# Kernel tuning notes

Hardware: AMD Instinct MI355X
Metric: run time of the kernel (lower is better)

## Reference

```python
import jax, jax.numpy as jnp
import numpy as np

BATCH, HID, STEPS = 64, 2048, 30

def setup_inputs() -> dict:
    key = jax.random.key(0)
    ks = jax.random.split(key, 7)
    s = 1.0 / np.sqrt(HID)  # pytorch LSTM/Linear init scale
    return {
        "monthly_token": jax.random.normal(ks[0], (BATCH, HID), jnp.float32),
        "steps": STEPS,
        "W_ih": jax.random.uniform(ks[1], (4 * HID, HID), jnp.float32, -s, s),
        "W_hh": jax.random.uniform(ks[2], (4 * HID, HID), jnp.float32, -s, s),
        "b_ih": jax.random.uniform(ks[3], (4 * HID,), jnp.float32, -s, s),
        "b_hh": jax.random.uniform(ks[4], (4 * HID,), jnp.float32, -s, s),
        "W_out": jax.random.uniform(ks[5], (1, HID), jnp.float32, -s, s),
        "b_out": jax.random.uniform(ks[6], (1,), jnp.float32, -s, s),
    }

def reference(monthly_token, steps, W_ih, W_hh, b_ih, b_hh, W_out, b_out):
    H = monthly_token.shape[1]
    h0 = monthly_token                      # (B, H) initial hidden
    c0 = jnp.zeros_like(h0)
    x0 = jnp.zeros_like(h0)                 # first lstm input is zeros

    def step(carry, _):
        h, c, x = carry
        # PyTorch gate order: input, forget, cell(g), output
        gates = x @ W_ih.T + b_ih + h @ W_hh.T + b_hh   # (B, 4H)
        i, f, g, o = jnp.split(gates, 4, axis=-1)
        i = jax.nn.sigmoid(i)
        f = jax.nn.sigmoid(f)
        g = jnp.tanh(g)
        o = jax.nn.sigmoid(o)
        c_new = f * c + i * g
        h_new = o * jnp.tanh(c_new)
        y = h_new @ W_out.T + b_out          # (B, 1) daily value
        # feedback: next input is the lstm output (= h_new for 1-layer LSTM)
        return (h_new, c_new, h_new), y[:, 0]

    _, ys = jax.lax.scan(step, (h0, c0, x0), xs=None, length=steps)
    return ys.T                               # (B, steps)
```

## Files before the change

### kernel.cpp

```cpp
#include <hip/hip_runtime.h>
#include <cmath>


#define HID   2048
#define BATCH 64
#define G4    8192
#define NCU   256
#define HGRP  (HID * BATCH / 8)
#define NFLAGS 512

typedef __attribute__((ext_vector_type(8))) _Float16 half8;
typedef __attribute__((ext_vector_type(4))) float f32x4;

#define LDS_BYTES 155648

__global__ void k_init(const float* __restrict__ token, const float* __restrict__ bih,
                       const float* __restrict__ bhh, half8* __restrict__ h0p,
                       float* __restrict__ bsum, unsigned* __restrict__ flags) {
    int g = blockIdx.x * 256 + threadIdx.x;
    int l = g & 63, nt = (g >> 6) & 3, kt = g >> 8;
    int n = nt * 16 + (l & 15);
    int k0 = kt * 32 + (l >> 4) * 8;
    const float4* ps = (const float4*)(token + (size_t)n * HID + k0);
    float4 a = ps[0], b = ps[1];
    half8 v;
    v[0]=(_Float16)a.x; v[1]=(_Float16)a.y; v[2]=(_Float16)a.z; v[3]=(_Float16)a.w;
    v[4]=(_Float16)b.x; v[5]=(_Float16)b.y; v[6]=(_Float16)b.z; v[7]=(_Float16)b.w;
    h0p[g] = v;
    if (g < G4) bsum[g] = bih[g] + bhh[g];
    if (g < NFLAGS) flags[g] = 0u;
}

__global__ __launch_bounds__(512, 2)
void k_lstm(const float* __restrict__ wih, const float* __restrict__ whh,
            const float* __restrict__ bsum, const float* __restrict__ wout,
            _Float16* __restrict__ hbuf,
            float* __restrict__ ypart,
            unsigned* __restrict__ flags, int steps) {
    extern __shared__ char smem[];
    half8* Wlds = (half8*)smem;
    f32x4* red4 = (f32x4*)(smem + 131072);

    const int tid  = threadIdx.x;
    const int blk  = blockIdx.x;
    const int lane = tid & 63;
    const int w    = tid >> 6;
    const int half = w & 1;
    const int ks   = w >> 1;
    const int q    = lane >> 4;
    const int col  = lane & 15;

    for (int idx = tid; idx < 2 * 64 * 64; idx += 512) {
        int l = idx & 63, kt = (idx >> 6) & 63, m2 = idx >> 12;
        int m = l & 15;
        int gate = m2 * 2 + (m >> 3);
        int row  = gate * HID + blk * 8 + (m & 7);
        int colw = kt * 32 + (l >> 4) * 8;
        const float4* p = (const float4*)(whh + (size_t)row * HID + colw);
        float4 a = p[0], b = p[1];
        half8 v;
        v[0]=(_Float16)a.x; v[1]=(_Float16)a.y; v[2]=(_Float16)a.z; v[3]=(_Float16)a.w;
        v[4]=(_Float16)b.x; v[5]=(_Float16)b.y; v[6]=(_Float16)b.z; v[7]=(_Float16)b.w;
        Wlds[idx] = v;
    }

    float biasA[4] = {0,0,0,0}, biasB[4] = {0,0,0,0}, wj4[4] = {0,0,0,0};
    float c4[4] = {0.0f, 0.0f, 0.0f, 0.0f};
    if (w < 2) {
        #pragma unroll
        for (int r = 0; r < 4; ++r) {
            int rA = 4 * q + r;
            int rB = 16 + 4 * q + r;
            biasA[r] = bsum[(rA >> 3) * HID + blk * 8 + (rA & 7)];
            biasB[r] = bsum[(rB >> 3) * HID + blk * 8 + (rB & 7)];
            wj4[r]   = wout[blk * 8 + (q & 1) * 4 + r];
        }
    }
    __syncthreads();

    for (int t = 0; t < steps; ++t) {
        if (t) {
            while (__hip_atomic_load(&flags[half * NCU + ks * 64 + lane],
                                     __ATOMIC_RELAXED, __HIP_MEMORY_SCOPE_AGENT)
                   < (unsigned)t)
                __builtin_amdgcn_s_sleep(1);
            asm volatile("" ::: "memory");
        }
        const half8* hp = (const half8*)(hbuf + (size_t)t * HID * BATCH);
        f32x4 a00 = {0,0,0,0}, a01 = {0,0,0,0}, a10 = {0,0,0,0}, a11 = {0,0,0,0};
        const int ktb = ks * 16;
        #pragma unroll
        for (int kk = 0; kk < 16; ++kk) {
            int kt = ktb + kk;
            half8 av0 = Wlds[(kt) * 64 + lane];
            half8 av1 = Wlds[(64 + kt) * 64 + lane];
            half8 b0  = hp[(kt * 4 + half * 2 + 0) * 64 + lane];
            half8 b1  = hp[(kt * 4 + half * 2 + 1) * 64 + lane];
            a00 = __builtin_amdgcn_mfma_f32_16x16x32_f16(av0, b0, a00, 0, 0, 0);
            a01 = __builtin_amdgcn_mfma_f32_16x16x32_f16(av0, b1, a01, 0, 0, 0);
            a10 = __builtin_amdgcn_mfma_f32_16x16x32_f16(av1, b0, a10, 0, 0, 0);
            a11 = __builtin_amdgcn_mfma_f32_16x16x32_f16(av1, b1, a11, 0, 0, 0);
        }
        if (ks == 1 || ks == 3) {
            int srow = (ks == 3 ? 2 : 0) + half;
            red4[(srow * 4 + 0) * 64 + lane] = a00;
            red4[(srow * 4 + 1) * 64 + lane] = a01;
            red4[(srow * 4 + 2) * 64 + lane] = a10;
            red4[(srow * 4 + 3) * 64 + lane] = a11;
        }
        __syncthreads();
        if (ks == 0) {
            int srow = half;
            a00 += red4[(srow * 4 + 0) * 64 + lane];
            a01 += red4[(srow * 4 + 1) * 64 + lane];
            a10 += red4[(srow * 4 + 2) * 64 + lane];
            a11 += red4[(srow * 4 + 3) * 64 + lane];
        } else if (ks == 2) {
            int srow = 2 + half;
            a00 += red4[(srow * 4 + 0) * 64 + lane];
            a01 += red4[(srow * 4 + 1) * 64 + lane];
            a10 += red4[(srow * 4 + 2) * 64 + lane];
            a11 += red4[(srow * 4 + 3) * 64 + lane];
            int sdst = 4 + half;
            red4[(sdst * 4 + 0) * 64 + lane] = a00;
            red4[(sdst * 4 + 1) * 64 + lane] = a01;
            red4[(sdst * 4 + 2) * 64 + lane] = a10;
            red4[(sdst * 4 + 3) * 64 + lane] = a11;
        }
        __syncthreads();
        if (w < 2) {
            int srow = 4 + half;
            a00 += red4[(srow * 4 + 0) * 64 + lane];
            a01 += red4[(srow * 4 + 1) * 64 + lane];
            a10 += red4[(srow * 4 + 2) * 64 + lane];
            a11 += red4[(srow * 4 + 3) * 64 + lane];
            #pragma unroll
            for (int r = 0; r < 4; ++r) {
                a00[r] += biasA[r]; a01[r] += biasA[r];
                a10[r] += biasB[r]; a11[r] += biasB[r];
            }
            float x00[4], x01[4], x10[4], x11[4];
            #pragma unroll
            for (int r = 0; r < 4; ++r) {
                x00[r] = __shfl_xor(a00[r], 32);
                x01[r] = __shfl_xor(a01[r], 32);
                x10[r] = __shfl_xor(a10[r], 32);
                x11[r] = __shfl_xor(a11[r], 32);
            }
            const bool lo = (lane < 32);
            float hv[4];
            #pragma unroll
            for (int r = 0; r < 4; ++r) {
                float gi = lo ? a00[r] : x01[r];
                float gf = lo ? x00[r] : a01[r];
                float gg = lo ? a10[r] : x11[r];
                float go = lo ? x10[r] : a11[r];
                float iv = 1.0f / (1.0f + __expf(-gi));
                float fv = 1.0f / (1.0f + __expf(-gf));
                float eg = __expf(2.0f * gg);
                float gv = 1.0f - 2.0f / (eg + 1.0f);
                float ov = 1.0f / (1.0f + __expf(-go));
                c4[r] = fv * c4[r] + iv * gv;
                float ec = __expf(2.0f * c4[r]);
                float th = 1.0f - 2.0f / (ec + 1.0f);
                hv[r] = ov * th;
            }
            if (t < steps - 1) {
                union { unsigned short us[4]; unsigned long long ull; } pk;
                #pragma unroll
                for (int r = 0; r < 4; ++r) {
                    _Float16 hf = (_Float16)hv[r];
                    pk.us[r] = *(unsigned short*)&hf;
                }
                const int nt = half * 2 + (q >> 1);
                const size_t g = (size_t)((blk >> 2) * 4 + nt) * 64
                               + (blk & 3) * 16 + col;
                unsigned long long* dst = (unsigned long long*)
                    (hbuf + (size_t)(t + 1) * HID * BATCH + g * 8) + (q & 1);
                __hip_atomic_store(dst, pk.ull, __ATOMIC_RELAXED,
                                   __HIP_MEMORY_SCOPE_AGENT);
                asm volatile("s_waitcnt vmcnt(0)" ::: "memory");
                if (lane == 0)
                    __hip_atomic_store(&flags[half * NCU + blk], (unsigned)(t + 1),
                                       __ATOMIC_RELAXED, __HIP_MEMORY_SCOPE_AGENT);
            }
            float yp = wj4[0] * hv[0] + wj4[1] * hv[1]
                     + wj4[2] * hv[2] + wj4[3] * hv[3];
            yp += __shfl_xor(yp, 16);
            if ((q & 1) == 0)
                ypart[((size_t)t * NCU + blk) * 64
                      + half * 32 + (q >> 1) * 16 + col] = yp;
        }
        if (t == 0) {
            for (int idx = tid; idx < 2 * 64 * 64; idx += 512) {
                int l = idx & 63, kt = (idx >> 6) & 63, m2 = idx >> 12;
                int m = l & 15;
                int gate = m2 * 2 + (m >> 3);
                int row  = gate * HID + blk * 8 + (m & 7);
                int colw = kt * 32 + (l >> 4) * 8;
                const float4* p = (const float4*)(wih + (size_t)row * HID + colw);
                float4 a = p[0], b = p[1];
                half8 v = Wlds[idx];
                v[0] = (_Float16)((float)v[0] + a.x); v[1] = (_Float16)((float)v[1] + a.y);
                v[2] = (_Float16)((float)v[2] + a.z); v[3] = (_Float16)((float)v[3] + a.w);
                v[4] = (_Float16)((float)v[4] + b.x); v[5] = (_Float16)((float)v[5] + b.y);
                v[6] = (_Float16)((float)v[6] + b.z); v[7] = (_Float16)((float)v[7] + b.w);
                Wlds[idx] = v;
            }
            __syncthreads();
        }
    }
}

__global__ __launch_bounds__(512)
void k_yout(const float* __restrict__ ypart, const float* __restrict__ bout,
            float* __restrict__ out, int steps) {
    __shared__ float red[8][64];
    int t = blockIdx.x;
    int tid = threadIdx.x;
    int b = tid & 63, ch = tid >> 6;
    const float* p = ypart + (size_t)t * NCU * 64 + b;
    float s = 0.0f;
    #pragma unroll 8
    for (int cu = ch * 32; cu < ch * 32 + 32; ++cu) s += p[(size_t)cu * 64];
    red[ch][b] = s;
    __syncthreads();
    if (tid < 64) {
        float r = bout[0];
        #pragma unroll
        for (int u = 0; u < 8; ++u) r += red[u][tid];
        out[(size_t)tid * steps + t] = r;
    }
}

extern "C" void kernel_launch(void* const* d_in, const int* in_sizes, int n_in,
                              void* d_out, int out_size, void* d_ws, size_t ws_size,
                              hipStream_t stream) {
    const float* token = (const float*)d_in[0];
    const float* wih   = (const float*)d_in[2];
    const float* whh   = (const float*)d_in[3];
    const float* bih   = (const float*)d_in[4];
    const float* bhh   = (const float*)d_in[5];
    const float* wout  = (const float*)d_in[6];
    const float* bout  = (const float*)d_in[7];
    float* out = (float*)d_out;
    const int steps = out_size / BATCH;

    char* ws = (char*)d_ws;
    size_t off = 0;
    auto carve = [&](size_t bytes) -> void* {
        void* p = ws + off;
        off = (off + bytes + 255) & ~(size_t)255;
        return p;
    };
    _Float16* hbuf  = (_Float16*)carve((size_t)(steps + 1) * HID * BATCH * 2);
    float*    bsum  = (float*)carve((size_t)G4 * 4);
    float*    ypart = (float*)carve((size_t)steps * NCU * 64 * 4);
    unsigned* flags = (unsigned*)carve(NFLAGS * 4);

    hipFuncSetAttribute(reinterpret_cast<const void*>(&k_lstm),
                        hipFuncAttributeMaxDynamicSharedMemorySize, LDS_BYTES);

    k_init<<<dim3(HGRP / 256), dim3(256), 0, stream>>>(
        token, bih, bhh, (half8*)hbuf, bsum, flags);

    k_lstm<<<dim3(NCU), dim3(512), LDS_BYTES, stream>>>(
        wih, whh, bsum, wout, hbuf, ypart, flags, steps);

    k_yout<<<dim3(steps), dim3(512), 0, stream>>>(ypart, bout, out, steps);
}
```

Baseline: 457.0 us.

## Double workgroup to 1024 threads with gate-interleaved rows and per-wave batch tiles

Raises the persistent LSTM kernel from 8 to 16 waves per block. Each wave now owns one 16-column batch tile, and the W_hh/W_ih rows are re-laid-out in LDS so the four gates of a hidden unit sit in adjacent accumulator rows. This removes the cross-half shuffles in the gate math, lets each wave prefetch all its h fragments before the MFMA loop, and spreads the step's work over more waves to cut per-step latency. In exchange the flag array doubles, more waves poll flags each step, and the h store becomes a shuffle-assembled 32-bit write per lane.

```diff
diff --git a/kernel.cpp b/kernel.cpp
--- a/kernel.cpp
+++ b/kernel.cpp
@@ -7,7 +7,7 @@
 #define G4    8192
 #define NCU   256
 #define HGRP  (HID * BATCH / 8)
-#define NFLAGS 512
+#define NFLAGS 1024
 
 typedef __attribute__((ext_vector_type(8))) _Float16 half8;
 typedef __attribute__((ext_vector_type(4))) float f32x4;
@@ -31,7 +31,7 @@
     if (g < NFLAGS) flags[g] = 0u;
 }
 
-__global__ __launch_bounds__(512, 2)
+__global__ __launch_bounds__(1024, 4)
 void k_lstm(const float* __restrict__ wih, const float* __restrict__ whh,
             const float* __restrict__ bsum, const float* __restrict__ wout,
             _Float16* __restrict__ hbuf,
@@ -45,16 +45,17 @@
     const int blk  = blockIdx.x;
     const int lane = tid & 63;
     const int w    = tid >> 6;
-    const int half = w & 1;
-    const int ks   = w >> 1;
+    const int nt   = w & 3;
+    const int ks   = w >> 2;
     const int q    = lane >> 4;
     const int col  = lane & 15;
 
-    for (int idx = tid; idx < 2 * 64 * 64; idx += 512) {
-        int l = idx & 63, kt = (idx >> 6) & 63, m2 = idx >> 12;
-        int m = l & 15;
-        int gate = m2 * 2 + (m >> 3);
-        int row  = gate * HID + blk * 8 + (m & 7);
+    for (int idx = tid; idx < 2 * 64 * 64; idx += 1024) {
+        int l = idx & 63, kt = (idx >> 6) & 63, mt = idx >> 12;
+        int m16  = l & 15;
+        int gate = m16 & 3;
+        int uloc = (mt ? 4 : 0) + (m16 >> 2);
+        int row  = gate * HID + blk * 8 + uloc;
         int colw = kt * 32 + (l >> 4) * 8;
         const float4* p = (const float4*)(whh + (size_t)row * HID + colw);
         float4 a = p[0], b = p[1];
@@ -64,139 +65,115 @@
         Wlds[idx] = v;
     }
 
-    float biasA[4] = {0,0,0,0}, biasB[4] = {0,0,0,0}, wj4[4] = {0,0,0,0};
-    float c4[4] = {0.0f, 0.0f, 0.0f, 0.0f};
-    if (w < 2) {
+    float bias0[4] = {0,0,0,0}, bias1[4] = {0,0,0,0};
+    float wj0 = 0.0f, wj1 = 0.0f, c20 = 0.0f, c21 = 0.0f;
+    if (ks == 0) {
         #pragma unroll
         for (int r = 0; r < 4; ++r) {
-            int rA = 4 * q + r;
-            int rB = 16 + 4 * q + r;
-            biasA[r] = bsum[(rA >> 3) * HID + blk * 8 + (rA & 7)];
-            biasB[r] = bsum[(rB >> 3) * HID + blk * 8 + (rB & 7)];
-            wj4[r]   = wout[blk * 8 + (q & 1) * 4 + r];
-        }
+            bias0[r] = bsum[r * HID + blk * 8 + q];
+            bias1[r] = bsum[r * HID + blk * 8 + 4 + q];
+        }
+        wj0 = wout[blk * 8 + q];
+        wj1 = wout[blk * 8 + 4 + q];
     }
     __syncthreads();
 
     for (int t = 0; t < steps; ++t) {
         if (t) {
-            while (__hip_atomic_load(&flags[half * NCU + ks * 64 + lane],
+            while (__hip_atomic_load(&flags[nt * NCU + ks * 64 + lane],
                                      __ATOMIC_RELAXED, __HIP_MEMORY_SCOPE_AGENT)
                    < (unsigned)t)
                 __builtin_amdgcn_s_sleep(1);
             asm volatile("" ::: "memory");
         }
         const half8* hp = (const half8*)(hbuf + (size_t)t * HID * BATCH);
-        f32x4 a00 = {0,0,0,0}, a01 = {0,0,0,0}, a10 = {0,0,0,0}, a11 = {0,0,0,0};
         const int ktb = ks * 16;
+        half8 bfr[16];
+        #pragma unroll
+        for (int kk = 0; kk < 16; ++kk)
+            bfr[kk] = hp[((ktb + kk) * 4 + nt) * 64 + lane];
+        __builtin_amdgcn_sched_barrier(0);
+        f32x4 a0 = {0,0,0,0}, a1 = {0,0,0,0};
         #pragma unroll
         for (int kk = 0; kk < 16; ++kk) {
             int kt = ktb + kk;
             half8 av0 = Wlds[(kt) * 64 + lane];
             half8 av1 = Wlds[(64 + kt) * 64 + lane];
-            half8 b0  = hp[(kt * 4 + half * 2 + 0) * 64 + lane];
-            half8 b1  = hp[(kt * 4 + half * 2 + 1) * 64 + lane];
-            a00 = __builtin_amdgcn_mfma_f32_16x16x32_f16(av0, b0, a00, 0, 0, 0);
-            a01 = __builtin_amdgcn_mfma_f32_16x16x32_f16(av0, b1, a01, 0, 0, 0);
-            a10 = __builtin_amdgcn_mfma_f32_16x16x32_f16(av1, b0, a10, 0, 0, 0);
-            a11 = __builtin_amdgcn_mfma_f32_16x16x32_f16(av1, b1, a11, 0, 0, 0);
-        }
-        if (ks == 1 || ks == 3) {
-            int srow = (ks == 3 ? 2 : 0) + half;
-            red4[(srow * 4 + 0) * 64 + lane] = a00;
-            red4[(srow * 4 + 1) * 64 + lane] = a01;
-            red4[(srow * 4 + 2) * 64 + lane] = a10;
-            red4[(srow * 4 + 3) * 64 + lane] = a11;
+            a0 = __builtin_amdgcn_mfma_f32_16x16x32_f16(av0, bfr[kk], a0, 0, 0, 0);
+            a1 = __builtin_amdgcn_mfma_f32_16x16x32_f16(av1, bfr[kk], a1, 0, 0, 0);
+        }
+        if (ks == 1) {
+            red4[(nt * 2 + 0) * 64 + lane] = a0;
+            red4[(nt * 2 + 1) * 64 + lane] = a1;
+        } else if (ks == 3) {
+            red4[(8 + nt * 2 + 0) * 64 + lane] = a0;
+            red4[(8 + nt * 2 + 1) * 64 + lane] = a1;
         }
         __syncthreads();
         if (ks == 0) {
-            int srow = half;
-            a00 += red4[(srow * 4 + 0) * 64 + lane];
-            a01 += red4[(srow * 4 + 1) * 64 + lane];
-            a10 += red4[(srow * 4 + 2) * 64 + lane];
-            a11 += red4[(srow * 4 + 3) * 64 + lane];
+            a0 += red4[(nt * 2 + 0) * 64 + lane];
+            a1 += red4[(nt * 2 + 1) * 64 + lane];
         } else if (ks == 2) {
-            int srow = 2 + half;
-            a00 += red4[(srow * 4 + 0) * 64 + lane];
-            a01 += red4[(srow * 4 + 1) * 64 + lane];
-            a10 += red4[(srow * 4 + 2) * 64 + lane];
-            a11 += red4[(srow * 4 + 3) * 64 + lane];
-            int sdst = 4 + half;
-            red4[(sdst * 4 + 0) * 64 + lane] = a00;
-            red4[(sdst * 4 + 1) * 64 + lane] = a01;
-            red4[(sdst * 4 + 2) * 64 + lane] = a10;
-            red4[(sdst * 4 + 3) * 64 + lane] = a11;
+            a0 += red4[(8 + nt * 2 + 0) * 64 + lane];
+            a1 += red4[(8 + nt * 2 + 1) * 64 + lane];
+            red4[(16 + nt * 2 + 0) * 64 + lane] = a0;
+            red4[(16 + nt * 2 + 1) * 64 + lane] = a1;
         }
         __syncthreads();
-        if (w < 2) {
-            int srow = 4 + half;
-            a00 += red4[(srow * 4 + 0) * 64 + lane];
-            a01 += red4[(srow * 4 + 1) * 64 + lane];
-            a10 += red4[(srow * 4 + 2) * 64 + lane];
-            a11 += red4[(srow * 4 + 3) * 64 + lane];
+        if (ks == 0) {
+            a0 += red4[(16 + nt * 2 + 0) * 64 + lane];
+            a1 += red4[(16 + nt * 2 + 1) * 64 + lane];
             #pragma unroll
-            for (int r = 0; r < 4; ++r) {
-                a00[r] += biasA[r]; a01[r] += biasA[r];
-                a10[r] += biasB[r]; a11[r] += biasB[r];
-            }
-            float x00[4], x01[4], x10[4], x11[4];
-            #pragma unroll
-            for (int r = 0; r < 4; ++r) {
-                x00[r] = __shfl_xor(a00[r], 32);
-                x01[r] = __shfl_xor(a01[r], 32);
-                x10[r] = __shfl_xor(a10[r], 32);
-                x11[r] = __shfl_xor(a11[r], 32);
-            }
-            const bool lo = (lane < 32);
-            float hv[4];
-            #pragma unroll
-            for (int r = 0; r < 4; ++r) {
-                float gi = lo ? a00[r] : x01[r];
-                float gf = lo ? x00[r] : a01[r];
-                float gg = lo ? a10[r] : x11[r];
-                float go = lo ? x10[r] : a11[r];
-                float iv = 1.0f / (1.0f + __expf(-gi));
-                float fv = 1.0f / (1.0f + __expf(-gf));
-                float eg = __expf(2.0f * gg);
-                float gv = 1.0f - 2.0f / (eg + 1.0f);
-                float ov = 1.0f / (1.0f + __expf(-go));
-                c4[r] = fv * c4[r] + iv * gv;
-                float ec = __expf(2.0f * c4[r]);
-                float th = 1.0f - 2.0f / (ec + 1.0f);
-                hv[r] = ov * th;
-            }
+            for (int r = 0; r < 4; ++r) { a0[r] += bias0[r]; a1[r] += bias1[r]; }
+            float iv0 = 1.0f / (1.0f + __expf(-a0[0]));
+            float fv0 = 1.0f / (1.0f + __expf(-a0[1]));
+            float gv0 = 1.0f - 2.0f / (__expf(2.0f * a0[2]) + 1.0f);
+            float ov0 = 1.0f / (1.0f + __expf(-a0[3]));
+            c20 = fv0 * c20 + iv0 * gv0;
+            float hv0 = ov0 * (1.0f - 2.0f / (__expf(2.0f * c20) + 1.0f));
+            float iv1 = 1.0f / (1.0f + __expf(-a1[0]));
+            float fv1 = 1.0f / (1.0f + __expf(-a1[1]));
+            float gv1 = 1.0f - 2.0f / (__expf(2.0f * a1[2]) + 1.0f);
+            float ov1 = 1.0f / (1.0f + __expf(-a1[3]));
+            c21 = fv1 * c21 + iv1 * gv1;
+            float hv1 = ov1 * (1.0f - 2.0f / (__expf(2.0f * c21) + 1.0f));
             if (t < steps - 1) {
-                union { unsigned short us[4]; unsigned long long ull; } pk;
-                #pragma unroll
-                for (int r = 0; r < 4; ++r) {
-                    _Float16 hf = (_Float16)hv[r];
-                    pk.us[r] = *(unsigned short*)&hf;
+                union { _Float16 h; unsigned short u; } u0, u1;
+                u0.h = (_Float16)hv0; u1.h = (_Float16)hv1;
+                unsigned m = ((unsigned)u1.u << 16) | u0.u;
+                unsigned x = __shfl_xor((int)m, 16);
+                unsigned val; int widx;
+                if ((q & 1) == 0) {
+                    val = ((x & 0xFFFFu) << 16) | (m & 0xFFFFu);
+                    widx = q >> 1;
+                } else {
+                    val = (m & 0xFFFF0000u) | (x >> 16);
+                    widx = 2 + (q >> 1);
                 }
-                const int nt = half * 2 + (q >> 1);
                 const size_t g = (size_t)((blk >> 2) * 4 + nt) * 64
                                + (blk & 3) * 16 + col;
-                unsigned long long* dst = (unsigned long long*)
-                    (hbuf + (size_t)(t + 1) * HID * BATCH + g * 8) + (q & 1);
-                __hip_atomic_store(dst, pk.ull, __ATOMIC_RELAXED,
+                unsigned* p32 = (unsigned*)
+                    (hbuf + (size_t)(t + 1) * HID * BATCH + g * 8);
+                __hip_atomic_store(p32 + widx, val, __ATOMIC_RELAXED,
                                    __HIP_MEMORY_SCOPE_AGENT);
                 asm volatile("s_waitcnt vmcnt(0)" ::: "memory");
                 if (lane == 0)
-                    __hip_atomic_store(&flags[half * NCU + blk], (unsigned)(t + 1),
+                    __hip_atomic_store(&flags[nt * NCU + blk], (unsigned)(t + 1),
                                        __ATOMIC_RELAXED, __HIP_MEMORY_SCOPE_AGENT);
             }
-            float yp = wj4[0] * hv[0] + wj4[1] * hv[1]
-                     + wj4[2] * hv[2] + wj4[3] * hv[3];
+            float yp = wj0 * hv0 + wj1 * hv1;
             yp += __shfl_xor(yp, 16);
-            if ((q & 1) == 0)
-                ypart[((size_t)t * NCU + blk) * 64
-                      + half * 32 + (q >> 1) * 16 + col] = yp;
+            yp += __shfl_xor(yp, 32);
+            if (lane < 16)
+                ypart[((size_t)t * NCU + blk) * 64 + nt * 16 + lane] = yp;
         }
         if (t == 0) {
-            for (int idx = tid; idx < 2 * 64 * 64; idx += 512) {
-                int l = idx & 63, kt = (idx >> 6) & 63, m2 = idx >> 12;
-                int m = l & 15;
-                int gate = m2 * 2 + (m >> 3);
-                int row  = gate * HID + blk * 8 + (m & 7);
+            for (int idx = tid; idx < 2 * 64 * 64; idx += 1024) {
+                int l = idx & 63, kt = (idx >> 6) & 63, mt = idx >> 12;
+                int m16  = l & 15;
+                int gate = m16 & 3;
+                int uloc = (mt ? 4 : 0) + (m16 >> 2);
+                int row  = gate * HID + blk * 8 + uloc;
                 int colw = kt * 32 + (l >> 4) * 8;
                 const float4* p = (const float4*)(wih + (size_t)row * HID + colw);
                 float4 a = p[0], b = p[1];
@@ -264,7 +241,7 @@
     k_init<<<dim3(HGRP / 256), dim3(256), 0, stream>>>(
         token, bih, bhh, (half8*)hbuf, bsum, flags);
 
-    k_lstm<<<dim3(NCU), dim3(512), LDS_BYTES, stream>>>(
+    k_lstm<<<dim3(NCU), dim3(1024), LDS_BYTES, stream>>>(
         wih, whh, bsum, wout, hbuf, ypart, flags, steps);
 
     k_yout<<<dim3(steps), dim3(512), 0, stream>>>(ypart, bout, out, steps);
```

Measured after the change: 490.4 us. 7.3% more time.
